# Kernel tuning notes

Hardware: AMD Instinct MI355X
Metric: run time of the kernel (lower is better)

The kernel has to match this reference:

```python
import jax, jax.numpy as jnp
import numpy as np

KH, KW = 3, 3
SH, SW = 1, 1
IC, OC = 32, 32
M = 4
P = M * M
ITERS = 3
LAM = 1.0
EPS = 1e-8


def _patches(t, kh, kw, sh, sw):
    # t: [B, H, W, ...] -> [B, Ho, Wo, kh, kw, ...] (im2col, matches torch unfold+permute)
    H, W = t.shape[1], t.shape[2]
    Ho = (H - kh) // sh + 1
    Wo = (W - kw) // sw + 1
    i = (jnp.arange(Ho) * sh)[:, None] + jnp.arange(kh)[None, :]  # [Ho,kh]
    j = (jnp.arange(Wo) * sw)[:, None] + jnp.arange(kw)[None, :]  # [Wo,kw]
    tp = t[:, i]            # [B,Ho,kh,W,...]
    tp = tp[:, :, :, j]     # [B,Ho,kh,Wo,kw,...]
    return jnp.moveaxis(tp, 2, 3)  # [B,Ho,Wo,kh,kw,...]


def setup_inputs() -> dict:
    key = jax.random.key(0)
    k1, k2, k3, k4, k5 = jax.random.split(key, 5)
    x = jax.random.normal(k1, (4, 14, 14, IC, M, M), dtype=jnp.float32)
    a = jax.random.uniform(k2, (4, 14, 14, IC), dtype=jnp.float32)
    W = jax.random.uniform(k3, (KH, KW, IC, OC, M, M), dtype=jnp.float32)   # torch.rand init
    beta_u = jax.random.uniform(k4, (1, OC, 1), dtype=jnp.float32)
    beta_a = jax.random.uniform(k5, (1, OC), dtype=jnp.float32)
    return {"x": x, "a": a, "W": W, "beta_u": beta_u, "beta_a": beta_a}


def reference(x, a, W, beta_u, beta_a):
    # im2col patches
    xp = _patches(x, KH, KW, SH, SW)          # [B,Ho,Wo,kh,kw,IC,M,M]
    ap = _patches(a, KH, KW, SH, SW)          # [B,Ho,Wo,kh,kw,IC]
    # pose-transform votes: per (kh,kw,inCap,outCap) 4x4 matmul
    V = jnp.einsum('bhwklcxy,klcoyz->bhwklcoxz', xp, W)
    B, Ho, Wo = V.shape[:3]
    N = KH * KW * IC
    V = V.reshape(B, Ho, Wo, N, OC, P)        # votes
    a_in = ap.reshape(B, Ho, Wo, N)
    bu = beta_u.reshape(OC, 1)
    ba = beta_a.reshape(OC)

    # EM routing (Hinton et al. 2018, fixed inverse temperature)
    R = jnp.full((B, Ho, Wo, N, OC), 1.0 / OC, dtype=V.dtype)
    for it in range(ITERS):
        Ra = R * a_in[..., None]                                  # [B,Ho,Wo,N,OC]
        Rs = Ra.sum(axis=3) + EPS                                 # [B,Ho,Wo,OC]
        mu = jnp.einsum('bhwno,bhwnop->bhwop', Ra, V) / Rs[..., None]
        d = V - mu[:, :, :, None]                                 # [B,Ho,Wo,N,OC,P]
        sig2 = jnp.einsum('bhwno,bhwnop->bhwop', Ra, d * d) / Rs[..., None] + EPS
        cost = (bu + 0.5 * jnp.log(sig2)) * Rs[..., None]         # [B,Ho,Wo,OC,P]
        a_out = jax.nn.sigmoid(LAM * (ba - cost.sum(-1)))         # [B,Ho,Wo,OC]
        if it < ITERS - 1:
            logp = -0.5 * jnp.sum(d * d / sig2[:, :, :, None] + jnp.log(sig2)[:, :, :, None], axis=-1)
            R = jax.nn.softmax(jnp.log(a_out + EPS)[:, :, :, None] + logp, axis=-1)

    pose = mu.reshape(B, Ho, Wo, OC, M, M)
    return pose, a_out
```

## Files before the change

kernel.cpp:

```cpp
#include <hip/hip_runtime.h>


#define EPSV 1e-8f

template <int CTRL>
__device__ __forceinline__ float dppf(float v) {
  return __int_as_float(__builtin_amdgcn_update_dpp(
      0, __float_as_int(v), CTRL, 0xf, 0xf, true));
}
__device__ __forceinline__ float swz16(float v) {
  return __int_as_float(__builtin_amdgcn_ds_swizzle(__float_as_int(v), 0x401F));
}
__device__ __forceinline__ float red_max32(float v) {
  v = fmaxf(v, dppf<0xB1>(v));
  v = fmaxf(v, dppf<0x4E>(v));
  v = fmaxf(v, dppf<0x141>(v));
  v = fmaxf(v, dppf<0x140>(v));
  v = fmaxf(v, swz16(v));
  return v;
}
__device__ __forceinline__ float red_sum32(float v) {
  v += dppf<0xB1>(v);
  v += dppf<0x4E>(v);
  v += dppf<0x141>(v);
  v += dppf<0x140>(v);
  v += swz16(v);
  return v;
}

__device__ __forceinline__ void compute_votes(const float* __restrict__ Wt,
                                              const float* __restrict__ xr,
                                              int n, int o, float* __restrict__ V)
{
  float Wf[16];
  {
    const float* wp = Wt + (((n << 5) + o) << 4);
#pragma unroll
    for (int i = 0; i < 4; ++i) {
      const float4 q = *(const float4*)(wp + (i << 2));
      Wf[i*4+0]=q.x; Wf[i*4+1]=q.y; Wf[i*4+2]=q.z; Wf[i*4+3]=q.w;
    }
  }
  float xv[16];
#pragma unroll
  for (int i = 0; i < 4; ++i) {
    const float4 q = *(const float4*)(xr + (i << 2));
    xv[i*4+0]=q.x; xv[i*4+1]=q.y; xv[i*4+2]=q.z; xv[i*4+3]=q.w;
  }
#pragma unroll
  for (int xi = 0; xi < 4; ++xi)
#pragma unroll
    for (int z = 0; z < 4; ++z)
      V[xi*4+z] = fmaf(xv[xi*4+0], Wf[z],
                  fmaf(xv[xi*4+1], Wf[4+z],
                  fmaf(xv[xi*4+2], Wf[8+z],
                       xv[xi*4+3]* Wf[12+z])));
}

__global__ __launch_bounds__(512, 4) void caps_stats(
    const float* __restrict__ X, const float* __restrict__ A, const float* __restrict__ Wt,
    const float* __restrict__ Bu, const float* __restrict__ Ba,
    const float* __restrict__ prev, float* __restrict__ cur, int it)
{
  __shared__ float xp_s[2*144*16];
  __shared__ float a_s[2*144];
  __shared__ float part[8*544];
  __shared__ float prs[8*32];

  const int t    = threadIdx.x;
  const int o    = t & 31;
  const int ng   = (t >> 5) & 7;
  const int ph   = t >> 8;
  const int wv   = t >> 6;
  const int lane = t & 63;

  const int bid   = blockIdx.x;
  const int pair  = bid >> 1;
  const int half  = bid & 1;
  const int nbase = half * 144;
  const int mypos = pair*2 + ph;

  for (int i = t; i < 1152; i += 512) {
    const int pp  = (i >= 576) ? 1 : 0;
    const int loc = i - pp*576;
    const int r   = loc >> 2, q4 = loc & 3;
    const int pos = pair*2 + pp;
    const int b = pos/144, r_ = pos - b*144, h = r_/12, w = r_ - (r_/12)*12;
    const int n = nbase + r;
    const int kl = n >> 5, c = n & 31;
    const int hy = h + kl/3, wx = w + (kl - (kl/3)*3);
    const float4 v = *(const float4*)(X + ((((b*14+hy)*14+wx) << 9) + (c << 4) + (q4 << 2)));
    *(float4*)(xp_s + pp*2304 + (r << 4) + (q4 << 2)) = v;
  }
  if (t < 288) {
    const int pp  = (t >= 144) ? 1 : 0;
    const int r   = t - pp*144;
    const int pos = pair*2 + pp;
    const int b = pos/144, r_ = pos - b*144, h = r_/12, w = r_ - (r_/12)*12;
    const int n = nbase + r;
    const int kl = n >> 5, c = n & 31;
    const int hy = h + kl/3, wx = w + (kl - (kl/3)*3);
    a_s[pp*144 + r] = A[((b*14+hy)*14+wx)*32 + c];
  }

  float mu_r[16], isig_r[16];
  float la_r = 0.f, slog_r = 0.f;
  if (it > 0) {
    const float* b0 = prev + (mypos*2 + 0)*1056;
    const float* b1 = prev + (mypos*2 + 1)*1056;
    float s1[16], s2[16];
#pragma unroll
    for (int k = 0; k < 4; ++k) {
      const float4 u0 = *(const float4*)(b0 + (o << 4) + (k << 2));
      const float4 u1 = *(const float4*)(b1 + (o << 4) + (k << 2));
      s1[k*4+0]=u0.x+u1.x; s1[k*4+1]=u0.y+u1.y; s1[k*4+2]=u0.z+u1.z; s1[k*4+3]=u0.w+u1.w;
      const float4 v0 = *(const float4*)(b0 + 512 + (o << 4) + (k << 2));
      const float4 v1 = *(const float4*)(b1 + 512 + (o << 4) + (k << 2));
      s2[k*4+0]=v0.x+v1.x; s2[k*4+1]=v0.y+v1.y; s2[k*4+2]=v0.z+v1.z; s2[k*4+3]=v0.w+v1.w;
    }
    const float rsum = b0[1024+o] + b1[1024+o] + EPSV;
    float slog = 0.f;
#pragma unroll
    for (int p = 0; p < 16; ++p) {
      const float mu = s1[p] / rsum;
      float var = s2[p] / rsum - mu*mu;
      var = fmaxf(var, 0.f);
      const float sg = var + EPSV;
      mu_r[p]   = mu;
      isig_r[p] = 1.0f / sg;
      slog     += __logf(sg);
    }
    const float cost = rsum * (16.0f*Bu[o] + 0.5f*slog);
    const float av = 1.0f / (1.0f + __expf(-(Ba[o] - cost)));
    la_r   = __logf(av + EPSV);
    slog_r = slog;
  } else {
#pragma unroll
    for (int p = 0; p < 16; ++p) { mu_r[p] = 0.f; isig_r[p] = 0.f; }
  }
  __syncthreads();

  float S1[16], S2[16];
#pragma unroll
  for (int p = 0; p < 16; ++p) { S1[p] = 0.f; S2[p] = 0.f; }
  float rs = 0.f;

#pragma unroll 1
  for (int j = 0; j < 18; ++j) {
    const int nl = ng + (j << 3);
    const int n  = nbase + nl;
    float V[16];
    compute_votes(Wt, xp_s + ph*2304 + (nl << 4), n, o, V);

    float ra;
    if (it == 0) {
      ra = a_s[ph*144 + nl] * (1.0f/32.0f);
    } else {
      float q0 = 0.f, q1 = 0.f, q2 = 0.f, q3 = 0.f;
#pragma unroll
      for (int p = 0; p < 4; ++p) {
        float d;
        d = V[p]    - mu_r[p];    q0 = fmaf(d*d, isig_r[p],    q0);
        d = V[p+4]  - mu_r[p+4];  q1 = fmaf(d*d, isig_r[p+4],  q1);
        d = V[p+8]  - mu_r[p+8];  q2 = fmaf(d*d, isig_r[p+8],  q2);
        d = V[p+12] - mu_r[p+12]; q3 = fmaf(d*d, isig_r[p+12], q3);
      }
      const float q = slog_r + ((q0 + q1) + (q2 + q3));
      const float z = la_r - 0.5f*q;
      const float m  = red_max32(z);
      const float ev = __expf(z - m);
      const float s  = red_sum32(ev);
      ra = (ev / s) * a_s[ph*144 + nl];
    }
    rs += ra;
#pragma unroll
    for (int p = 0; p < 16; ++p) {
      const float rv = ra * V[p];
      S1[p] += rv;
      S2[p] = fmaf(rv, V[p], S2[p]);
    }
  }

#pragma unroll
  for (int p = 0; p < 16; ++p) {
    S1[p] += __shfl_xor(S1[p], 32);
    S2[p] += __shfl_xor(S2[p], 32);
  }
  rs += __shfl_xor(rs, 32);

  float* seg0 = cur + ((pair*2 + 0)*2 + half)*1056;
  float* seg1 = cur + ((pair*2 + 1)*2 + half)*1056;

  if (lane < 32) {
    float* p1 = part + wv*544 + o*17;
#pragma unroll
    for (int p = 0; p < 16; ++p) p1[p] = S1[p];
    prs[wv*32 + o] = rs;
  }
  __syncthreads();
  for (int c = t; c < 1024; c += 512) {
    const int pc = c >> 9, idx = c & 511;
    const int pi = idx >> 5, oo = idx & 31;
    float s = 0.f;
#pragma unroll
    for (int g = 0; g < 4; ++g) s += part[(pc*4 + g)*544 + oo*17 + pi];
    (pc ? seg1 : seg0)[(oo << 4) + pi] = s;
  }
  if (t < 64) {
    const int pc = t >> 5, oo = t & 31;
    float r = 0.f;
#pragma unroll
    for (int g = 0; g < 4; ++g) r += prs[(pc*4 + g)*32 + oo];
    (pc ? seg1 : seg0)[1024 + oo] = r;
  }
  __syncthreads();

  if (lane < 32) {
    float* p2 = part + wv*544 + o*17;
#pragma unroll
    for (int p = 0; p < 16; ++p) p2[p] = S2[p];
  }
  __syncthreads();
  for (int c = t; c < 1024; c += 512) {
    const int pc = c >> 9, idx = c & 511;
    const int pi = idx >> 5, oo = idx & 31;
    float s = 0.f;
#pragma unroll
    for (int g = 0; g < 4; ++g) s += part[(pc*4 + g)*544 + oo*17 + pi];
    (pc ? seg1 : seg0)[512 + (oo << 4) + pi] = s;
  }
}

__global__ __launch_bounds__(512, 4) void caps_final(
    const float* __restrict__ prev, const float* __restrict__ Bu,
    const float* __restrict__ Ba, float* __restrict__ Out)
{
  __shared__ float lsig_t[512];
  __shared__ float rs_s[32], aout_s[32];

  const int t   = threadIdx.x;
  const int pos = blockIdx.x;
  const float* h0 = prev + (pos*2 + 0)*1056;
  const float* h1 = prev + (pos*2 + 1)*1056;

  const int oo = t >> 4;
  const float rsum = h0[1024+oo] + h1[1024+oo] + EPSV;
  const float s1 = h0[t]     + h1[t];
  const float s2 = h0[512+t] + h1[512+t];
  const float mu = s1 / rsum;
  float var = s2 / rsum - mu*mu;
  var = fmaxf(var, 0.f);
  lsig_t[t] = __logf(var + EPSV);
  if ((t & 15) == 0) rs_s[oo] = rsum;
  __syncthreads();
  if (t < 32) {
    float slog = 0.f;
#pragma unroll
    for (int p = 0; p < 16; ++p) slog += lsig_t[(t << 4) + p];
    const float cost = rs_s[t] * (16.0f*Bu[t] + 0.5f*slog);
    aout_s[t] = 1.0f / (1.0f + __expf(-(Ba[t] - cost)));
  }
  __syncthreads();
  Out[pos*512 + t] = mu;
  if (t < 32) Out[294912 + pos*32 + t] = aout_s[t];
}

extern "C" void kernel_launch(void* const* d_in, const int* in_sizes, int n_in,
                              void* d_out, int out_size, void* d_ws, size_t ws_size,
                              hipStream_t stream) {
  (void)in_sizes; (void)n_in; (void)ws_size; (void)out_size;
  const float* X  = (const float*)d_in[0];
  const float* A  = (const float*)d_in[1];
  const float* Wt = (const float*)d_in[2];
  const float* Bu = (const float*)d_in[3];
  const float* Ba = (const float*)d_in[4];
  float* Out = (float*)d_out;

  float* pa = (float*)d_ws;
  float* pb = pa + 1152*1056;

  hipLaunchKernelGGL(caps_stats, dim3(576), dim3(512), 0, stream,
                     X, A, Wt, Bu, Ba, (const float*)nullptr, pa, 0);
  hipLaunchKernelGGL(caps_stats, dim3(576), dim3(512), 0, stream,
                     X, A, Wt, Bu, Ba, pa, pb, 1);
  hipLaunchKernelGGL(caps_stats, dim3(576), dim3(512), 0, stream,
                     X, A, Wt, Bu, Ba, pb, pa, 2);
  hipLaunchKernelGGL(caps_final, dim3(576), dim3(512), 0, stream,
                     pa, Bu, Ba, Out);
}
```

Baseline: 191.9 us.

## Compute routing stats cooperatively in shared memory and remap threads per wave

The per-thread recomputation of mu, inverse sigma and activation from the previous partial sums is replaced by a block-cooperative pass: each thread handles one (capsule, pose) element, reduces the log-sums with DPP, and stores the results in shared memory for every thread to read back. Thread mapping changes so each wave holds both positions (ph from the lane) and iterates over n-groups by wave index. This removes the cross-half shuffle reduction, and the final reduction becomes four phases summing eight partials. It costs extra shared memory and more barriers in the epilogue, which may lower occupancy.

```diff
diff --git a/kernel.cpp b/kernel.cpp
--- a/kernel.cpp
+++ b/kernel.cpp
@@ -27,6 +27,13 @@
   v += swz16(v);
   return v;
 }
+__device__ __forceinline__ float red_sum16(float v) {
+  v += dppf<0xB1>(v);
+  v += dppf<0x4E>(v);
+  v += dppf<0x141>(v);
+  v += dppf<0x140>(v);
+  return v;
+}
 
 __device__ __forceinline__ void compute_votes(const float* __restrict__ Wt,
                                               const float* __restrict__ xr,
@@ -62,23 +69,24 @@
     const float* __restrict__ Bu, const float* __restrict__ Ba,
     const float* __restrict__ prev, float* __restrict__ cur, int it)
 {
-  __shared__ float xp_s[2*144*16];
-  __shared__ float a_s[2*144];
-  __shared__ float part[8*544];
-  __shared__ float prs[8*32];
+  __shared__ float  xp_s[2*144*16];
+  __shared__ float  a_s[2*144];
+  __shared__ float  part[8*544];
+  __shared__ float  prs[8*32];
+  __shared__ float2 misg_s[2*512];
+  __shared__ float  la_s[64];
+  __shared__ float  slog_s[64];
 
   const int t    = threadIdx.x;
-  const int o    = t & 31;
-  const int ng   = (t >> 5) & 7;
-  const int ph   = t >> 8;
+  const int lane = t & 63;
+  const int o    = lane & 31;
+  const int ph   = lane >> 5;
   const int wv   = t >> 6;
-  const int lane = t & 63;
 
   const int bid   = blockIdx.x;
   const int pair  = bid >> 1;
   const int half  = bid & 1;
   const int nbase = half * 144;
-  const int mypos = pair*2 + ph;
 
   for (int i = t; i < 1152; i += 512) {
     const int pp  = (i >= 576) ? 1 : 0;
@@ -103,42 +111,47 @@
     a_s[pp*144 + r] = A[((b*14+hy)*14+wx)*32 + c];
   }
 
+  if (it > 0) {
+    const int oo = t >> 4, pi = t & 15;
+#pragma unroll
+    for (int pp = 0; pp < 2; ++pp) {
+      const float* h0 = prev + ((pair*2 + pp)*2 + 0)*1056;
+      const float* h1 = prev + ((pair*2 + pp)*2 + 1)*1056;
+      const float s1   = h0[t]       + h1[t];
+      const float s2   = h0[512 + t] + h1[512 + t];
+      const float rsum = h0[1024+oo] + h1[1024+oo] + EPSV;
+      const float mu = s1 / rsum;
+      float var = s2 / rsum - mu*mu;
+      var = fmaxf(var, 0.f);
+      const float sg = var + EPSV;
+      const float lg = __logf(sg);
+      misg_s[pp*512 + pi*32 + oo] = make_float2(mu, 1.0f / sg);
+      const float sl = red_sum16(lg);
+      if (pi == 0) {
+        const float cost = rsum * (16.0f*Bu[oo] + 0.5f*sl);
+        const float av = 1.0f / (1.0f + __expf(-(Ba[oo] - cost)));
+        la_s[pp*32 + oo]   = __logf(av + EPSV);
+        slog_s[pp*32 + oo] = sl;
+      }
+    }
+  }
+  __syncthreads();
+
   float mu_r[16], isig_r[16];
   float la_r = 0.f, slog_r = 0.f;
   if (it > 0) {
-    const float* b0 = prev + (mypos*2 + 0)*1056;
-    const float* b1 = prev + (mypos*2 + 1)*1056;
-    float s1[16], s2[16];
-#pragma unroll
-    for (int k = 0; k < 4; ++k) {
-      const float4 u0 = *(const float4*)(b0 + (o << 4) + (k << 2));
-      const float4 u1 = *(const float4*)(b1 + (o << 4) + (k << 2));
-      s1[k*4+0]=u0.x+u1.x; s1[k*4+1]=u0.y+u1.y; s1[k*4+2]=u0.z+u1.z; s1[k*4+3]=u0.w+u1.w;
-      const float4 v0 = *(const float4*)(b0 + 512 + (o << 4) + (k << 2));
-      const float4 v1 = *(const float4*)(b1 + 512 + (o << 4) + (k << 2));
-      s2[k*4+0]=v0.x+v1.x; s2[k*4+1]=v0.y+v1.y; s2[k*4+2]=v0.z+v1.z; s2[k*4+3]=v0.w+v1.w;
-    }
-    const float rsum = b0[1024+o] + b1[1024+o] + EPSV;
-    float slog = 0.f;
 #pragma unroll
     for (int p = 0; p < 16; ++p) {
-      const float mu = s1[p] / rsum;
-      float var = s2[p] / rsum - mu*mu;
-      var = fmaxf(var, 0.f);
-      const float sg = var + EPSV;
-      mu_r[p]   = mu;
-      isig_r[p] = 1.0f / sg;
-      slog     += __logf(sg);
-    }
-    const float cost = rsum * (16.0f*Bu[o] + 0.5f*slog);
-    const float av = 1.0f / (1.0f + __expf(-(Ba[o] - cost)));
-    la_r   = __logf(av + EPSV);
-    slog_r = slog;
+      const float2 ms = misg_s[ph*512 + p*32 + o];
+      mu_r[p]   = ms.x;
+      isig_r[p] = ms.y;
+    }
+    la_r   = la_s[ph*32 + o];
+    slog_r = slog_s[ph*32 + o];
   } else {
 #pragma unroll
     for (int p = 0; p < 16; ++p) { mu_r[p] = 0.f; isig_r[p] = 0.f; }
   }
-  __syncthreads();
 
   float S1[16], S2[16];
 #pragma unroll
@@ -147,7 +160,7 @@
 
 #pragma unroll 1
   for (int j = 0; j < 18; ++j) {
-    const int nl = ng + (j << 3);
+    const int nl = wv + (j << 3);
     const int n  = nbase + nl;
     float V[16];
     compute_votes(Wt, xp_s + ph*2304 + (nl << 4), n, o, V);
@@ -181,53 +194,40 @@
     }
   }
 
-#pragma unroll
-  for (int p = 0; p < 16; ++p) {
-    S1[p] += __shfl_xor(S1[p], 32);
-    S2[p] += __shfl_xor(S2[p], 32);
-  }
-  rs += __shfl_xor(rs, 32);
-
   float* seg0 = cur + ((pair*2 + 0)*2 + half)*1056;
   float* seg1 = cur + ((pair*2 + 1)*2 + half)*1056;
 
-  if (lane < 32) {
-    float* p1 = part + wv*544 + o*17;
-#pragma unroll
-    for (int p = 0; p < 16; ++p) p1[p] = S1[p];
-    prs[wv*32 + o] = rs;
-  }
-  __syncthreads();
-  for (int c = t; c < 1024; c += 512) {
-    const int pc = c >> 9, idx = c & 511;
-    const int pi = idx >> 5, oo = idx & 31;
-    float s = 0.f;
-#pragma unroll
-    for (int g = 0; g < 4; ++g) s += part[(pc*4 + g)*544 + oo*17 + pi];
-    (pc ? seg1 : seg0)[(oo << 4) + pi] = s;
-  }
-  if (t < 64) {
-    const int pc = t >> 5, oo = t & 31;
-    float r = 0.f;
-#pragma unroll
-    for (int g = 0; g < 4; ++g) r += prs[(pc*4 + g)*32 + oo];
-    (pc ? seg1 : seg0)[1024 + oo] = r;
-  }
-  __syncthreads();
-
-  if (lane < 32) {
-    float* p2 = part + wv*544 + o*17;
-#pragma unroll
-    for (int p = 0; p < 16; ++p) p2[p] = S2[p];
-  }
-  __syncthreads();
-  for (int c = t; c < 1024; c += 512) {
-    const int pc = c >> 9, idx = c & 511;
-    const int pi = idx >> 5, oo = idx & 31;
-    float s = 0.f;
-#pragma unroll
-    for (int g = 0; g < 4; ++g) s += part[(pc*4 + g)*544 + oo*17 + pi];
-    (pc ? seg1 : seg0)[512 + (oo << 4) + pi] = s;
+#pragma unroll
+  for (int phase = 0; phase < 4; ++phase) {
+    const int  wp  = phase & 1;
+    const bool s2p = phase >= 2;
+    if (ph == wp) {
+      float* pw = part + wv*544 + o*17;
+      if (!s2p) {
+#pragma unroll
+        for (int p = 0; p < 16; ++p) pw[p] = S1[p];
+        prs[wv*32 + o] = rs;
+      } else {
+#pragma unroll
+        for (int p = 0; p < 16; ++p) pw[p] = S2[p];
+      }
+    }
+    __syncthreads();
+    {
+      const int oo = t >> 4, pi = t & 15;
+      float s = 0.f;
+#pragma unroll
+      for (int g = 0; g < 8; ++g) s += part[g*544 + oo*17 + pi];
+      float* seg = wp ? seg1 : seg0;
+      seg[(s2p ? 512 : 0) + t] = s;
+      if (!s2p && t < 32) {
+        float r = 0.f;
+#pragma unroll
+        for (int g = 0; g < 8; ++g) r += prs[(g << 5) + t];
+        seg[1024 + t] = r;
+      }
+    }
+    __syncthreads();
   }
 }
 
@@ -240,10 +240,10 @@
 
   const int t   = threadIdx.x;
   const int pos = blockIdx.x;
+  const int oo  = t >> 4;
   const float* h0 = prev + (pos*2 + 0)*1056;
   const float* h1 = prev + (pos*2 + 1)*1056;
 
-  const int oo = t >> 4;
   const float rsum = h0[1024+oo] + h1[1024+oo] + EPSV;
   const float s1 = h0[t]     + h1[t];
   const float s2 = h0[512+t] + h1[512+t];
```

Result: faster. 174.9 us (-8.9%).
